# Optimization experiments

Hardware: AMD Instinct MI355X
Metric: run time of the kernel (lower is better)

Reference implementation:

```python
import jax, jax.numpy as jnp
import numpy as np

OUT, IN, GS = 11008, 4096, 128   # out_features, in_features, group_size
G = IN // GS                     # num_groups = 32 (in_features divisible by group_size)
TOKENS = 8192                    # batch 4 * seq 2048


def setup_inputs() -> dict:
    key = jax.random.key(0)
    k1, k2, k3, k4, k5 = jax.random.split(key, 5)
    x = jax.random.normal(k1, (TOKENS, IN), dtype=jnp.float32)
    # packed int4 weights: two nibbles per byte, stored as int32 in [0,256)
    qweight = jax.random.randint(k2, (OUT, IN // 2), 0, 256, dtype=jnp.int32)
    # realistic GPTQ scales (small positive) and zero-points in [0,15]
    scales = jax.random.uniform(k3, (OUT, G), dtype=jnp.float32) * 0.01 + 1e-3
    zeros = jax.random.uniform(k4, (OUT, G), dtype=jnp.float32) * 15.0
    bias = jax.random.normal(k5, (OUT,), dtype=jnp.float32) * 0.01
    return {"x": x, "qweight": qweight, "scales": scales, "zeros": zeros, "bias": bias}


def _dequant(qweight, scales, zeros):
    # unpack: column 2i = low nibble, column 2i+1 = high nibble (matches torch loop)
    low = (qweight & 15).astype(jnp.float32)          # [OUT, IN/2]
    high = ((qweight >> 4) & 15).astype(jnp.float32)  # [OUT, IN/2]
    w = jnp.stack([low, high], axis=-1).reshape(OUT, IN)
    # group-wise dequant: (q - zero) * scale per group of GS input channels
    w = (w.reshape(OUT, G, GS) - zeros[:, :, None]) * scales[:, :, None]
    return w.reshape(OUT, IN)


def reference(x, qweight, scales, zeros, bias):
    w = _dequant(qweight, scales, zeros)   # [OUT, IN] fp32
    # F.linear: x @ w.T + bias
    return jnp.einsum('ti,oi->to', x, w) + bias
```

## Files before the change

kernel.cpp:

```cpp
#include <hip/hip_runtime.h>
#include <stdint.h>

#define OUTF 11008
#define INF  4096
#define NG   32
#define TOK  8192
#define KB4  2048

#define BM 128
#define BN 256
#define BK 32
#define NT (INF / BK)
#define GX (OUTF / BN)
#define GY (TOK / BM)
#define NWG (GX * GY)

typedef unsigned short u16;
typedef __attribute__((ext_vector_type(8))) short bf16x8;
typedef __attribute__((ext_vector_type(4))) float f32x4;
typedef __attribute__((ext_vector_type(16))) float f32x16;
typedef __attribute__((ext_vector_type(4))) int i32x4;

__device__ inline u16 f2bf(float f) {
  union { float f; uint32_t u; } v; v.f = f;
  return (u16)((v.u + 0x7fff + ((v.u >> 16) & 1)) >> 16);
}

__device__ inline void async_copy16(const void* g, const void* l) {
  __builtin_amdgcn_global_load_lds(
      (__attribute__((address_space(1))) void*)(g),
      (__attribute__((address_space(3))) void*)(l), 16, 0, 0);
}

#define FENCE() asm volatile("" ::: "memory")
#define BAR()   do { FENCE(); __builtin_amdgcn_s_barrier(); FENCE(); } while (0)
#define VMCNT(n) asm volatile("s_waitcnt vmcnt(" #n ")" ::: "memory")


#define NXU ((long long)TOK * INF / 4)
#define NWU ((long long)OUTF * KB4 / 4)
#define PREPBLK 2048

__global__ __launch_bounds__(256) void prep(const float* __restrict__ X,
                                            const int* __restrict__ QW,
                                            const float* __restrict__ scales,
                                            const float* __restrict__ zeros,
                                            u16* __restrict__ Xb,
                                            u16* __restrict__ Wb) {
  const long long stride = (long long)gridDim.x * 256;
  for (long long i = (long long)blockIdx.x * 256 + threadIdx.x; i < NXU + NWU;
       i += stride) {
    if (i < NXU) {
      const f32x4 f = __builtin_nontemporal_load((const f32x4*)X + i);
      union { u16 t[4]; uint2 v; } u;
      u.t[0] = f2bf(f[0]); u.t[1] = f2bf(f[1]);
      u.t[2] = f2bf(f[2]); u.t[3] = f2bf(f[3]);
      ((uint2*)Xb)[i] = u.v;
    } else {
      const long long j = i - NXU;
      const int o = (int)(j >> 9);
      const int c0 = ((int)j & 511) * 4;
      const int g = c0 >> 6;
      const float s = scales[o * NG + g];
      const float zs = -zeros[o * NG + g] * s;
      const i32x4 q = __builtin_nontemporal_load((const i32x4*)QW + j);
      union { u16 t[8]; int4 v; } u;
#pragma unroll
      for (int k = 0; k < 4; ++k) {
        u.t[2 * k]     = f2bf(fmaf((float)(q[k] & 15), s, zs));
        u.t[2 * k + 1] = f2bf(fmaf((float)((q[k] >> 4) & 15), s, zs));
      }
      ((int4*)Wb)[j] = u.v;
    }
  }
}


__global__ __launch_bounds__(512, 4) void gemm_occ(const u16* __restrict__ A,
                                                   const u16* __restrict__ B,
                                                   const float* __restrict__ bias,
                                                   float* __restrict__ C) {
  __shared__ __align__(16) u16 As[2][BM * BK];
  __shared__ __align__(16) u16 Bs[2][BN * BK];
  const int tid = threadIdx.x;
  const int lane = tid & 63;
  const int wid = __builtin_amdgcn_readfirstlane(tid >> 6);

  const int lin = blockIdx.x;
  const int xcd = lin & 7;
  const int wgc = lin >> 3;
  int bmr, bn;
  if (wgc < 320) {
    const int g = wgc >> 6, r = wgc & 63;
    bn = g * 8 + (r & 7);
    bmr = r >> 3;
  } else {
    const int r = wgc - 320;
    bn = 40 + r % 3;
    bmr = r / 3;
  }
  const int bm = xcd * 8 + bmr;

  const u16* Ab = A + (size_t)bm * BM * INF;
  const u16* Bb = B + (size_t)bn * BN * INF;

  const int rowoff = tid >> 2;
  const int gran = (tid & 3) ^ ((rowoff >> 1) & 3) ^ ((rowoff >> 3) & 3);
  const u16* Asrc = Ab + (size_t)rowoff * INF + gran * 8;
  const u16* Bsrc = Bb + (size_t)rowoff * INF + gran * 8;

  const int rr32 = lane & 31;
  const int hi = lane >> 5;
  const int xr2 = ((rr32 >> 1) & 3) ^ ((rr32 >> 3) & 3);
  const int wm = wid >> 2;
  const int wn = wid & 3;

  f32x16 acc[2][2] = {};

#define STG(LDS, SRC, TT, R0)                                                  \
  async_copy16((SRC) + (size_t)(R0) * INF + (size_t)(TT) * BK,                 \
               (const char*)(LDS) + (R0) * 64 + wid * 1024);

#define RD_ALL(S)                                                              \
  _Pragma("unroll") for (int mt = 0; mt < 2; ++mt)                             \
    _Pragma("unroll") for (int ks = 0; ks < 2; ++ks)                           \
      af[mt][ks] = *(const bf16x8*)&As[S][                                     \
          (wm * 64 + mt * 32 + rr32) * BK + (((ks * 2 + hi) ^ xr2) * 8)];      \
  _Pragma("unroll") for (int nt = 0; nt < 2; ++nt)                             \
    _Pragma("unroll") for (int ks = 0; ks < 2; ++ks)                           \
      bf[nt][ks] = *(const bf16x8*)&Bs[S][                                     \
          (wn * 64 + nt * 32 + rr32) * BK + (((ks * 2 + hi) ^ xr2) * 8)];

#define MFMA_ALL()                                                             \
  do {                                                                         \
    __builtin_amdgcn_s_setprio(1);                                             \
    _Pragma("unroll") for (int ks = 0; ks < 2; ++ks)                           \
      _Pragma("unroll") for (int mt = 0; mt < 2; ++mt)                         \
        _Pragma("unroll") for (int nt = 0; nt < 2; ++nt)                       \
          acc[mt][nt] = __builtin_amdgcn_mfma_f32_32x32x16_bf16(               \
              af[mt][ks], bf[nt][ks], acc[mt][nt], 0, 0, 0);                   \
    __builtin_amdgcn_s_setprio(0);                                             \
  } while (0)

  STG(&As[0][0], Asrc, 0, 0)
  STG(&Bs[0][0], Bsrc, 0, 0) STG(&Bs[0][0], Bsrc, 0, 128)
  STG(&As[1][0], Asrc, 1, 0)
  STG(&Bs[1][0], Bsrc, 1, 0) STG(&Bs[1][0], Bsrc, 1, 128)
  VMCNT(3);
  BAR();

  for (int t = 0; t < NT; ++t) {
    const int S = t & 1;
    bf16x8 af[2][2], bf[2][2];
    RD_ALL(S);
    MFMA_ALL();
    BAR();
    if (t + 2 < NT) {
      STG(&As[S][0], Asrc, t + 2, 0)
      STG(&Bs[S][0], Bsrc, t + 2, 0) STG(&Bs[S][0], Bsrc, t + 2, 128)
      VMCNT(3);
    } else {
      VMCNT(0);
    }
    BAR();
  }

  float bv[2];
#pragma unroll
  for (int nt = 0; nt < 2; ++nt)
    bv[nt] = bias[bn * BN + wn * 64 + nt * 32 + rr32];
#pragma unroll
  for (int mt = 0; mt < 2; ++mt)
#pragma unroll
    for (int nt = 0; nt < 2; ++nt) {
      const int gn = bn * BN + wn * 64 + nt * 32 + rr32;
#pragma unroll
      for (int reg = 0; reg < 16; ++reg) {
        const int gm = bm * BM + wm * 64 + mt * 32 +
                       (reg & 3) + 8 * (reg >> 2) + 4 * hi;
        __builtin_nontemporal_store(acc[mt][nt][reg] + bv[nt],
                                    &C[(size_t)gm * OUTF + gn]);
      }
    }
}


#define FBM 128
#define FBN 128
#define FBK 64

#define FMFMA_COMPUTE()                                                       \
  do {                                                                        \
    const int frr = lane & 15;                                                \
    const int fq4 = lane >> 4;                                                \
    _Pragma("unroll") for (int ks = 0; ks < 2; ++ks) {                        \
      bf16x8 fa[4], fb[4];                                                    \
      const int kk = (((ks * 4 + fq4) ^ (frr & 7)) * 8);                      \
      _Pragma("unroll") for (int i = 0; i < 4; ++i) {                         \
        fa[i] = *(const bf16x8*)&Asf[(mwave + i * 16 + frr) * FBK + kk];      \
        fb[i] = *(const bf16x8*)&Bsf[(nwave + i * 16 + frr) * FBK + kk];      \
      }                                                                       \
      _Pragma("unroll") for (int mi = 0; mi < 4; ++mi)                        \
        _Pragma("unroll") for (int ni = 0; ni < 4; ++ni)                      \
          facc[mi][ni] = __builtin_amdgcn_mfma_f32_16x16x32_bf16(             \
              fa[mi], fb[ni], facc[mi][ni], 0, 0, 0);                         \
    }                                                                         \
  } while (0)

__global__ __launch_bounds__(256) void gemm_fused(const float* __restrict__ X,
                                                  const int* __restrict__ QW,
                                                  const float* __restrict__ scales,
                                                  const float* __restrict__ zeros,
                                                  const float* __restrict__ bias,
                                                  float* __restrict__ C) {
  __shared__ __align__(16) u16 Asf[FBM * FBK];
  __shared__ __align__(16) u16 Bsf[FBN * FBK];
  const int tid = threadIdx.x;
  const int lane = tid & 63;
  const int wid = tid >> 6;
  const int bm = blockIdx.y, bn = blockIdx.x;
  const int row = tid >> 1;
  const int half = tid & 1;
  const float* xr = X + (size_t)(bm * FBM + row) * INF + half * 32;
  const int* qr = QW + (size_t)(bn * FBN + row) * KB4 + half * 16;
  const float* srow = scales + (size_t)(bn * FBN + row) * NG;
  const float* zrow = zeros + (size_t)(bn * FBN + row) * NG;
  const int mwave = (wid >> 1) * 64;
  const int nwave = (wid & 1) * 64;
  f32x4 facc[4][4] = {};

  for (int kb = 0; kb < INF / FBK; ++kb) {
    const int k0 = kb * FBK;
    union { u16 t[32]; int4 v[4]; } ta, tb;
#pragma unroll
    for (int j = 0; j < 8; ++j) {
      const float4 f = *(const float4*)(xr + k0 + j * 4);
      ta.t[4 * j]     = f2bf(f.x);
      ta.t[4 * j + 1] = f2bf(f.y);
      ta.t[4 * j + 2] = f2bf(f.z);
      ta.t[4 * j + 3] = f2bf(f.w);
    }
    {
      const float s = srow[kb >> 1];
      const float zs = -zrow[kb >> 1] * s;
#pragma unroll
      for (int j = 0; j < 4; ++j) {
        const int4 q = *(const int4*)(qr + kb * 32 + j * 4);
        const int qq[4] = {q.x, q.y, q.z, q.w};
#pragma unroll
        for (int u = 0; u < 4; ++u) {
          tb.t[8 * j + 2 * u]     = f2bf(fmaf((float)(qq[u] & 15), s, zs));
          tb.t[8 * j + 2 * u + 1] = f2bf(fmaf((float)((qq[u] >> 4) & 15), s, zs));
        }
      }
    }
    __syncthreads();
#pragma unroll
    for (int j = 0; j < 4; ++j) {
      *(int4*)&Asf[row * FBK + (((half * 4 + j) ^ (row & 7)) * 8)] = ta.v[j];
      *(int4*)&Bsf[row * FBK + (((half * 4 + j) ^ (row & 7)) * 8)] = tb.v[j];
    }
    __syncthreads();
    FMFMA_COMPUTE();
  }
  {
    const int ncol = lane & 15;
    const int qrow = (lane >> 4) * 4;
#pragma unroll
    for (int mi = 0; mi < 4; ++mi)
#pragma unroll
      for (int ni = 0; ni < 4; ++ni) {
        const int gn = bn * FBN + nwave + ni * 16 + ncol;
        const float bvv = bias[gn];
#pragma unroll
        for (int r = 0; r < 4; ++r) {
          const int gm = bm * FBM + mwave + mi * 16 + qrow + r;
          C[(size_t)gm * OUTF + gn] = facc[mi][ni][r] + bvv;
        }
      }
  }
}


extern "C" void kernel_launch(void* const* d_in, const int* in_sizes, int n_in,
                              void* d_out, int out_size, void* d_ws, size_t ws_size,
                              hipStream_t stream) {
  const float* x = (const float*)d_in[0];
  const int* qw = (const int*)d_in[1];
  const float* scales = (const float*)d_in[2];
  const float* zeros = (const float*)d_in[3];
  const float* bias = (const float*)d_in[4];
  float* out = (float*)d_out;

  const size_t needW = (size_t)OUTF * INF * sizeof(u16);
  const size_t needX = (size_t)TOK * INF * sizeof(u16);

  if (ws_size >= needW + needX) {
    u16* Wb = (u16*)d_ws;
    u16* Xb = (u16*)((char*)d_ws + needW);
    prep<<<PREPBLK, 256, 0, stream>>>(x, qw, scales, zeros, Xb, Wb);
    gemm_occ<<<dim3(NWG), 512, 0, stream>>>(Xb, Wb, bias, out);
  } else {
    gemm_fused<<<dim3(OUTF / FBN, TOK / FBM), 256, 0, stream>>>(x, qw, scales, zeros, bias, out);
  }
}
```

Before: 1.216 ms.

## Double GEMM K-tile to 64 and single-buffer the A tile

Raises the K tile depth from 32 to 64 so the main loop runs half as many iterations and half as many barrier pairs. The XOR swizzle and LDS addressing are reworked for 128-byte rows, and the MFMA work is split into four k-group phases per tile. The A tile now uses a single LDS buffer loaded one step ahead, while B stays double-buffered two steps ahead. The A load for the next tile is waited on right after it is issued, so its latency is not hidden behind compute. LDS use per block also rises from 48 KB to 80 KB, which can lower how many blocks fit on a CU.

```diff
diff --git a/kernel.cpp b/kernel.cpp
--- a/kernel.cpp
+++ b/kernel.cpp
@@ -9,7 +9,7 @@
 
 #define BM 128
 #define BN 256
-#define BK 32
+#define BK 64
 #define NT (INF / BK)
 #define GX (OUTF / BN)
 #define GY (TOK / BM)
@@ -76,11 +76,11 @@
 }
 
 
-__global__ __launch_bounds__(512, 4) void gemm_occ(const u16* __restrict__ A,
-                                                   const u16* __restrict__ B,
-                                                   const float* __restrict__ bias,
-                                                   float* __restrict__ C) {
-  __shared__ __align__(16) u16 As[2][BM * BK];
+__global__ __launch_bounds__(512, 4) void gemm_occ2(const u16* __restrict__ A,
+                                                    const u16* __restrict__ B,
+                                                    const float* __restrict__ bias,
+                                                    float* __restrict__ C) {
+  __shared__ __align__(16) u16 As[BM * BK];
   __shared__ __align__(16) u16 Bs[2][BN * BK];
   const int tid = threadIdx.x;
   const int lane = tid & 63;
@@ -104,61 +104,62 @@
   const u16* Ab = A + (size_t)bm * BM * INF;
   const u16* Bb = B + (size_t)bn * BN * INF;
 
-  const int rowoff = tid >> 2;
-  const int gran = (tid & 3) ^ ((rowoff >> 1) & 3) ^ ((rowoff >> 3) & 3);
+  const int rowoff = tid >> 3;
+  const int gran = (tid & 7) ^ (rowoff & 7) ^ ((rowoff >> 3) & 3);
   const u16* Asrc = Ab + (size_t)rowoff * INF + gran * 8;
   const u16* Bsrc = Bb + (size_t)rowoff * INF + gran * 8;
+  const int wid8 = wid * 8;
 
   const int rr32 = lane & 31;
   const int hi = lane >> 5;
-  const int xr2 = ((rr32 >> 1) & 3) ^ ((rr32 >> 3) & 3);
+  const int xr = (rr32 & 7) ^ ((rr32 >> 3) & 3);
   const int wm = wid >> 2;
   const int wn = wid & 3;
 
   f32x16 acc[2][2] = {};
 
-#define STG(LDS, SRC, TT, R0)                                                  \
+#define STAGE1(LDS, SRC, TT, R0)                                               \
   async_copy16((SRC) + (size_t)(R0) * INF + (size_t)(TT) * BK,                 \
-               (const char*)(LDS) + (R0) * 64 + wid * 1024);
-
-#define RD_ALL(S)                                                              \
+               (const char*)(LDS) + ((R0) + wid8) * 128);
+
+#define RD_A2(DST, KG)                                                         \
   _Pragma("unroll") for (int mt = 0; mt < 2; ++mt)                             \
-    _Pragma("unroll") for (int ks = 0; ks < 2; ++ks)                           \
-      af[mt][ks] = *(const bf16x8*)&As[S][                                     \
-          (wm * 64 + mt * 32 + rr32) * BK + (((ks * 2 + hi) ^ xr2) * 8)];      \
+    DST[mt] = *(const bf16x8*)&As[(wm * 64 + mt * 32 + rr32) * BK +            \
+                                  ((((KG) * 2 + hi) ^ xr) * 8)];
+#define RD_B2(DST, S, KG)                                                      \
   _Pragma("unroll") for (int nt = 0; nt < 2; ++nt)                             \
-    _Pragma("unroll") for (int ks = 0; ks < 2; ++ks)                           \
-      bf[nt][ks] = *(const bf16x8*)&Bs[S][                                     \
-          (wn * 64 + nt * 32 + rr32) * BK + (((ks * 2 + hi) ^ xr2) * 8)];
-
-#define MFMA_ALL()                                                             \
+    DST[nt] = *(const bf16x8*)&Bs[S][(wn * 64 + nt * 32 + rr32) * BK +         \
+                                     ((((KG) * 2 + hi) ^ xr) * 8)];
+
+#define KGPHASE(S, KG)                                                         \
   do {                                                                         \
+    bf16x8 af[2], bf[2];                                                       \
+    RD_A2(af, KG) RD_B2(bf, S, KG)                                             \
     __builtin_amdgcn_s_setprio(1);                                             \
-    _Pragma("unroll") for (int ks = 0; ks < 2; ++ks)                           \
-      _Pragma("unroll") for (int mt = 0; mt < 2; ++mt)                         \
-        _Pragma("unroll") for (int nt = 0; nt < 2; ++nt)                       \
-          acc[mt][nt] = __builtin_amdgcn_mfma_f32_32x32x16_bf16(               \
-              af[mt][ks], bf[nt][ks], acc[mt][nt], 0, 0, 0);                   \
+    _Pragma("unroll") for (int mt = 0; mt < 2; ++mt)                           \
+      _Pragma("unroll") for (int nt = 0; nt < 2; ++nt)                         \
+        acc[mt][nt] = __builtin_amdgcn_mfma_f32_32x32x16_bf16(                 \
+            af[mt], bf[nt], acc[mt][nt], 0, 0, 0);                             \
     __builtin_amdgcn_s_setprio(0);                                             \
   } while (0)
 
-  STG(&As[0][0], Asrc, 0, 0)
-  STG(&Bs[0][0], Bsrc, 0, 0) STG(&Bs[0][0], Bsrc, 0, 128)
-  STG(&As[1][0], Asrc, 1, 0)
-  STG(&Bs[1][0], Bsrc, 1, 0) STG(&Bs[1][0], Bsrc, 1, 128)
-  VMCNT(3);
+  STAGE1(&As[0], Asrc, 0, 0)      STAGE1(&As[0], Asrc, 0, 64)
+  STAGE1(&Bs[0][0], Bsrc, 0, 0)   STAGE1(&Bs[0][0], Bsrc, 0, 64)
+  STAGE1(&Bs[0][0], Bsrc, 0, 128) STAGE1(&Bs[0][0], Bsrc, 0, 192)
+  STAGE1(&Bs[1][0], Bsrc, 1, 0)   STAGE1(&Bs[1][0], Bsrc, 1, 64)
+  STAGE1(&Bs[1][0], Bsrc, 1, 128) STAGE1(&Bs[1][0], Bsrc, 1, 192)
+  VMCNT(4);
   BAR();
 
   for (int t = 0; t < NT; ++t) {
     const int S = t & 1;
-    bf16x8 af[2][2], bf[2][2];
-    RD_ALL(S);
-    MFMA_ALL();
+    KGPHASE(S, 0); KGPHASE(S, 1); KGPHASE(S, 2); KGPHASE(S, 3);
     BAR();
+    if (t + 1 < NT) { STAGE1(&As[0], Asrc, t + 1, 0) STAGE1(&As[0], Asrc, t + 1, 64) }
     if (t + 2 < NT) {
-      STG(&As[S][0], Asrc, t + 2, 0)
-      STG(&Bs[S][0], Bsrc, t + 2, 0) STG(&Bs[S][0], Bsrc, t + 2, 128)
-      VMCNT(3);
+      STAGE1(&Bs[S][0], Bsrc, t + 2, 0)   STAGE1(&Bs[S][0], Bsrc, t + 2, 64)
+      STAGE1(&Bs[S][0], Bsrc, t + 2, 128) STAGE1(&Bs[S][0], Bsrc, t + 2, 192)
+      VMCNT(4);
     } else {
       VMCNT(0);
     }
@@ -299,7 +300,7 @@
     u16* Wb = (u16*)d_ws;
     u16* Xb = (u16*)((char*)d_ws + needW);
     prep<<<PREPBLK, 256, 0, stream>>>(x, qw, scales, zeros, Xb, Wb);
-    gemm_occ<<<dim3(NWG), 512, 0, stream>>>(Xb, Wb, bias, out);
+    gemm_occ2<<<dim3(NWG), 512, 0, stream>>>(Xb, Wb, bias, out);
   } else {
     gemm_fused<<<dim3(OUTF / FBN, TOK / FBM), 256, 0, stream>>>(x, qw, scales, zeros, bias, out);
   }
```

Measured after the change: 1.125 ms. -7.5%, faster.
